# Performance work log

Hardware: AMD Instinct MI355X
Metric: run time of the kernel (lower is better)

Reference implementation:

```python
import jax, jax.numpy as jnp
import numpy as np

N, F_IN, F_OUT = 8192, 512, 64
LEAKY_ALPHA = 0.2
NEG_MASK = -9e15


def setup_inputs() -> dict:
    key = jax.random.key(0)
    k1, k2, k3, k4 = jax.random.split(key, 4)
    x = jax.random.normal(k1, (N, F_IN), dtype=jnp.float32)
    adj = jax.random.randint(k2, (N, N), 0, 2, dtype=jnp.int32)
    # xavier-normal-ish scale for params
    W = jax.random.normal(k3, (F_IN, F_OUT), dtype=jnp.float32) * np.sqrt(2.0 / (F_IN + F_OUT)).astype(np.float32)
    a = jax.random.normal(k4, (2 * F_OUT, 1), dtype=jnp.float32) * np.sqrt(2.0 / (2 * F_OUT + 1)).astype(np.float32)
    return {"x": x, "adj": adj, "W": W, "a": a}


def reference(x, adj, W, a):
    # eval mode: dropout is identity
    Wh = x @ W                                   # [N, F_out]
    wh_i = Wh @ a[:F_OUT, :]                     # [N, 1]
    wh_j = Wh @ a[F_OUT:, :]                     # [N, 1]
    e = wh_i + wh_j.T                            # [N, N] broadcast add
    e = jnp.where(e >= 0, e, LEAKY_ALPHA * e)    # leaky_relu
    e = jnp.where(adj > 0, e, NEG_MASK)
    attn = jax.nn.softmax(e, axis=1)             # row-wise softmax
    h = attn @ Wh                                # [N, F_out]
    # ELU activation
    return jax.nn.elu(h)
```

## Files before the change

### kernel.cpp

```cpp
#include <hip/hip_runtime.h>

#define NN 8192
#define FIN 512
#define FO 64

typedef short bf16x8 __attribute__((ext_vector_type(8)));
typedef float f32x4 __attribute__((ext_vector_type(4)));

union AFrag { bf16x8 v; __bf16 b[8]; };

__device__ __forceinline__ unsigned spread8(unsigned u) {
    u = (u | (u << 12)) & 0x000F000Fu;
    u = (u | (u << 6))  & 0x03030303u;
    u = (u | (u << 3))  & 0x11111111u;
    return u;
}

__global__ __launch_bounds__(512) void wt_kernel(const float* __restrict__ W, __bf16* __restrict__ WT) {
    __shared__ float tile[64][65];
    const int k0 = blockIdx.x * 64;
    #pragma unroll
    for (int r = 0; r < 8; ++r) {
        const int kl = r * 8 + (threadIdx.x >> 6);
        const int f  = threadIdx.x & 63;
        tile[kl][f] = W[(size_t)(k0 + kl) * FO + f];
    }
    __syncthreads();
    const int f   = threadIdx.x >> 3;
    const int kk8 = (threadIdx.x & 7) * 8;
    unsigned u[4];
    #pragma unroll
    for (int h = 0; h < 4; ++h) {
        union { __bf16 b; unsigned short us; } lo, hi;
        lo.b = (__bf16)tile[kk8 + 2*h][f];
        hi.b = (__bf16)tile[kk8 + 2*h + 1][f];
        u[h] = (unsigned)lo.us | ((unsigned)hi.us << 16);
    }
    *(uint4*)(WT + (size_t)f * FIN + k0 + kk8) = make_uint4(u[0], u[1], u[2], u[3]);
}

__global__ __launch_bounds__(128) void wh_kernel(
    const float* __restrict__ x, const __bf16* __restrict__ WT,
    const float* __restrict__ a, uint4* __restrict__ whs,
    float* __restrict__ s_out, float* __restrict__ t_out)
{
    __shared__ float whlds[2][16][FO + 1];
    const int w  = threadIdx.x >> 6;
    const int l  = threadIdx.x & 63;
    const int lr = l & 15, lg = l >> 4;
    const int rb = (blockIdx.x * 2 + w) * 16;

    f32x4 acc[4] = {};
    const float* xr = x + (size_t)(rb + lr) * FIN;
    const __bf16* wbase[4];
    #pragma unroll
    for (int ft = 0; ft < 4; ++ft) wbase[ft] = WT + (ft*16 + lr) * FIN;

    float4 nxa = *(const float4*)(xr + lg*4);
    float4 nxb = *(const float4*)(xr + lg*4 + 16);
    for (int ks = 0; ks < 16; ++ks) {
        const int k0 = ks*32 + lg*4;
        const float4 xa = nxa, xb = nxb;
        const int kn = (ks < 15 ? ks + 1 : 15)*32 + lg*4;
        nxa = *(const float4*)(xr + kn);
        nxb = *(const float4*)(xr + kn + 16);
        AFrag af;
        af.b[0]=(__bf16)xa.x; af.b[1]=(__bf16)xa.y; af.b[2]=(__bf16)xa.z; af.b[3]=(__bf16)xa.w;
        af.b[4]=(__bf16)xb.x; af.b[5]=(__bf16)xb.y; af.b[6]=(__bf16)xb.z; af.b[7]=(__bf16)xb.w;
        #pragma unroll
        for (int ft = 0; ft < 4; ++ft) {
            union { bf16x8 v; uint2 q[2]; } bf;
            bf.q[0] = *(const uint2*)(wbase[ft] + k0);
            bf.q[1] = *(const uint2*)(wbase[ft] + k0 + 16);
            acc[ft] = __builtin_amdgcn_mfma_f32_16x16x32_bf16(af.v, bf.v, acc[ft], 0, 0, 0);
        }
    }

    #pragma unroll
    for (int ft = 0; ft < 4; ++ft)
        #pragma unroll
        for (int q = 0; q < 4; ++q)
            whlds[w][lg*4+q][ft*16+lr] = acc[ft][q];

    float sp[4] = {0,0,0,0}, tp[4] = {0,0,0,0};
    #pragma unroll
    for (int ft = 0; ft < 4; ++ft) {
        const float a1 = a[ft*16 + lr];
        const float a2 = a[FO + ft*16 + lr];
        #pragma unroll
        for (int q = 0; q < 4; ++q) { sp[q] += acc[ft][q]*a1; tp[q] += acc[ft][q]*a2; }
    }
    #pragma unroll
    for (int d = 1; d < 16; d <<= 1) {
        #pragma unroll
        for (int q = 0; q < 4; ++q) { sp[q] += __shfl_xor(sp[q], d); tp[q] += __shfl_xor(tp[q], d); }
    }
    if (lr == 0) {
        *(float4*)(s_out + rb + lg*4) = make_float4(sp[0], sp[1], sp[2], sp[3]);
        *(float4*)(t_out + rb + lg*4) = make_float4(tp[0], tp[1], tp[2], tp[3]);
    }

    __syncthreads();

    const int jb = blockIdx.x;
    #pragma unroll
    for (int q = 0; q < 2; ++q) {
        const int ft = w*2 + q;
        const int f  = ft*16 + lr;
        unsigned u[4];
        #pragma unroll
        for (int h = 0; h < 4; ++h) {
            const int c0 = ((h & 2) ? 16 : 0) + lg*4 + (h & 1)*2;
            union { __bf16 b; unsigned short us; } lo, hi;
            lo.b = (__bf16)whlds[c0 >> 4][c0 & 15][f];
            hi.b = (__bf16)whlds[(c0+1) >> 4][(c0+1) & 15][f];
            u[h] = (unsigned)lo.us | ((unsigned)hi.us << 16);
        }
        whs[(jb*4 + ft)*64 + l] = make_uint4(u[0], u[1], u[2], u[3]);
    }
}

__global__ __launch_bounds__(256) void mask_kernel(
    const int* __restrict__ adj, unsigned* __restrict__ mask)
{
    const int l   = threadIdx.x & 63;
    const int wid = (blockIdx.x * 256 + threadIdx.x) >> 6;
    const int lsh = (l & 7) * 8;
    #pragma unroll 2
    for (int g = wid; g < NN * 32; g += 16384) {
        const int4 v = *(const int4*)(adj + (size_t)g * 256 + l * 4);
        const unsigned long long b0 = __ballot(v.x != 0);
        const unsigned long long b1 = __ballot(v.y != 0);
        const unsigned long long b2 = __ballot(v.z != 0);
        const unsigned long long b3 = __ballot(v.w != 0);
        if (l < 8) {
            const unsigned w0 = spread8((unsigned)(b0 >> lsh) & 0xFFu);
            const unsigned w1 = spread8((unsigned)(b1 >> lsh) & 0xFFu);
            const unsigned w2 = spread8((unsigned)(b2 >> lsh) & 0xFFu);
            const unsigned w3 = spread8((unsigned)(b3 >> lsh) & 0xFFu);
            mask[(size_t)g * 8 + l] = w0 | (w1 << 1) | (w2 << 2) | (w3 << 3);
        }
    }
}

__global__ __launch_bounds__(1024, 4) void gat3_kernel(
    const unsigned* __restrict__ mask, const uint4* __restrict__ whs,
    const float* __restrict__ s_in, const float* __restrict__ t_in,
    float* __restrict__ out)
{
    __shared__ float red[8][2048];
    __shared__ float dnl[16][32];
    __shared__ float dns[32];
    const int w  = threadIdx.x >> 6;
    const int l  = threadIdx.x & 63;
    const int lr = l & 15, lg = l >> 4;
    const int rg = blockIdx.x;
    const int r0 = rg * 32;
    const float sA = s_in[r0 + lr];
    const float sB = s_in[r0 + 16 + lr];
    const unsigned* mrowA = mask + (size_t)(r0 + lr) * 256;
    const unsigned* mrowB = mask + (size_t)(r0 + 16 + lr) * 256;
    const int sh0 = lg * 4;
    const bf16x8* wv = (const bf16x8*)whs;

    f32x4 acc[2][4] = {};
    float dnA = 0.f, dnB = 0.f;

    unsigned mA = mrowA[w*16], mB = mrowB[w*16];
    float4 t0 = *(const float4*)(t_in + w*512 + sh0);
    float4 t1 = *(const float4*)(t_in + w*512 + 16 + sh0);

    for (int it = 0; it < 16; ++it) {
        const int jb = w*16 + it;
        bf16x8 bv0 = wv[(jb*4 + 0)*64 + l];
        bf16x8 bv1 = wv[(jb*4 + 1)*64 + l];
        bf16x8 bv2 = wv[(jb*4 + 2)*64 + l];
        bf16x8 bv3 = wv[(jb*4 + 3)*64 + l];
        const int jn = w*16 + (it + 1 < 16 ? it + 1 : 15);
        const unsigned nmA = mrowA[jn], nmB = mrowB[jn];
        const float4 nt0 = *(const float4*)(t_in + jn*32 + sh0);
        const float4 nt1 = *(const float4*)(t_in + jn*32 + 16 + sh0);

        const float tv[8] = {t0.x, t0.y, t0.z, t0.w, t1.x, t1.y, t1.z, t1.w};
        AFrag afA, afB;
        #pragma unroll
        for (int e = 0; e < 8; ++e) {
            const int bit = (e < 4) ? (sh0 + e) : (12 + sh0 + e);
            float eA = sA + tv[e]; eA = fmaxf(eA, 0.2f * eA);
            float eB = sB + tv[e]; eB = fmaxf(eB, 0.2f * eB);
            const float pA = ((mA >> bit) & 1u) ? __expf(eA) : 0.f;
            const float pB = ((mB >> bit) & 1u) ? __expf(eB) : 0.f;
            dnA += pA; dnB += pB;
            afA.b[e] = (__bf16)pA;
            afB.b[e] = (__bf16)pB;
        }
        acc[0][0] = __builtin_amdgcn_mfma_f32_16x16x32_bf16(afA.v, bv0, acc[0][0], 0, 0, 0);
        acc[0][1] = __builtin_amdgcn_mfma_f32_16x16x32_bf16(afA.v, bv1, acc[0][1], 0, 0, 0);
        acc[0][2] = __builtin_amdgcn_mfma_f32_16x16x32_bf16(afA.v, bv2, acc[0][2], 0, 0, 0);
        acc[0][3] = __builtin_amdgcn_mfma_f32_16x16x32_bf16(afA.v, bv3, acc[0][3], 0, 0, 0);
        acc[1][0] = __builtin_amdgcn_mfma_f32_16x16x32_bf16(afB.v, bv0, acc[1][0], 0, 0, 0);
        acc[1][1] = __builtin_amdgcn_mfma_f32_16x16x32_bf16(afB.v, bv1, acc[1][1], 0, 0, 0);
        acc[1][2] = __builtin_amdgcn_mfma_f32_16x16x32_bf16(afB.v, bv2, acc[1][2], 0, 0, 0);
        acc[1][3] = __builtin_amdgcn_mfma_f32_16x16x32_bf16(afB.v, bv3, acc[1][3], 0, 0, 0);

        mA = nmA; mB = nmB; t0 = nt0; t1 = nt1;
    }

    dnA += __shfl_xor(dnA, 16); dnA += __shfl_xor(dnA, 32);
    dnB += __shfl_xor(dnB, 16); dnB += __shfl_xor(dnB, 32);
    if (l < 16) { dnl[w][l] = dnA; dnl[w][16 + l] = dnB; }
    __syncthreads();
    if (threadIdx.x < 32) {
        float s = 0.f;
        #pragma unroll
        for (int ww = 0; ww < 16; ++ww) s += dnl[ww][threadIdx.x];
        dns[threadIdx.x] = s;
    }

    for (int h = 8; h >= 1; h >>= 1) {
        if (w >= h && w < 2*h) {
            #pragma unroll
            for (int g = 0; g < 2; ++g)
                #pragma unroll
                for (int ft = 0; ft < 4; ++ft)
                    #pragma unroll
                    for (int q = 0; q < 4; ++q)
                        red[w - h][((g*16 + lg*4 + q)*FO) + ft*16 + lr] = acc[g][ft][q];
        }
        __syncthreads();
        if (w < h) {
            #pragma unroll
            for (int g = 0; g < 2; ++g)
                #pragma unroll
                for (int ft = 0; ft < 4; ++ft)
                    #pragma unroll
                    for (int q = 0; q < 4; ++q)
                        acc[g][ft][q] += red[w][((g*16 + lg*4 + q)*FO) + ft*16 + lr];
        }
        __syncthreads();
    }

    if (w == 0) {
        #pragma unroll
        for (int g = 0; g < 2; ++g) {
            #pragma unroll
            for (int ft = 0; ft < 4; ++ft) {
                #pragma unroll
                for (int q = 0; q < 4; ++q) {
                    const int m = g*16 + lg*4 + q;
                    const float h2 = acc[g][ft][q] / dns[m];
                    out[(size_t)(r0 + m) * FO + ft*16 + lr] =
                        (h2 > 0.f) ? h2 : (__expf(h2) - 1.f);
                }
            }
        }
    }
}

extern "C" void kernel_launch(void* const* d_in, const int* in_sizes, int n_in,
                              void* d_out, int out_size, void* d_ws, size_t ws_size,
                              hipStream_t stream) {
    const float* x   = (const float*)d_in[0];
    const int*   adj = (const int*)d_in[1];
    const float* W   = (const float*)d_in[2];
    const float* a   = (const float*)d_in[3];
    float* out = (float*)d_out;

    char* ws = (char*)d_ws;
    uint4*    whs  = (uint4*)ws;
    __bf16*   WT   = (__bf16*)(ws + (1u << 20));
    float*    s    = (float*)(ws + (1u << 20) + (1u << 16));
    float*    t    = (float*)(ws + (1u << 20) + (1u << 16) + 32768);
    unsigned* mask = (unsigned*)(ws + (2u << 20));

    wt_kernel  <<<8,    512, 0, stream>>>(W, WT);
    wh_kernel  <<<256,  128, 0, stream>>>(x, WT, a, whs, s, t);
    mask_kernel<<<4096, 256, 0, stream>>>(adj, mask);
    gat3_kernel<<<256, 1024, 0, stream>>>(mask, whs, s, t, out);
}
```

Measured before the change: 100.5 us.

## Fuse W transpose, Wh projection and adjacency mask packing into one launch

Removes the separate W-transpose kernel and merges the Wh GEMM kernel and the adj-to-bitmask kernel into one grid. The first 128 blocks compute Wh with 4 waves each, reading W directly from fp32 global memory and converting it to bf16 on the fly. The remaining 4096 blocks pack the mask, so the two independent stages overlap and two launches disappear. In exchange, the GEMM now does strided scalar W loads instead of vectorised loads of a pre-transposed bf16 copy.

Result: faster. 89.77 us (-10.6%).

```diff
diff --git a/kernel.cpp b/kernel.cpp
--- a/kernel.cpp
+++ b/kernel.cpp
@@ -16,45 +16,43 @@
     return u;
 }
 
-__global__ __launch_bounds__(512) void wt_kernel(const float* __restrict__ W, __bf16* __restrict__ WT) {
-    __shared__ float tile[64][65];
-    const int k0 = blockIdx.x * 64;
-    #pragma unroll
-    for (int r = 0; r < 8; ++r) {
-        const int kl = r * 8 + (threadIdx.x >> 6);
-        const int f  = threadIdx.x & 63;
-        tile[kl][f] = W[(size_t)(k0 + kl) * FO + f];
-    }
-    __syncthreads();
-    const int f   = threadIdx.x >> 3;
-    const int kk8 = (threadIdx.x & 7) * 8;
-    unsigned u[4];
-    #pragma unroll
-    for (int h = 0; h < 4; ++h) {
-        union { __bf16 b; unsigned short us; } lo, hi;
-        lo.b = (__bf16)tile[kk8 + 2*h][f];
-        hi.b = (__bf16)tile[kk8 + 2*h + 1][f];
-        u[h] = (unsigned)lo.us | ((unsigned)hi.us << 16);
-    }
-    *(uint4*)(WT + (size_t)f * FIN + k0 + kk8) = make_uint4(u[0], u[1], u[2], u[3]);
-}
-
-__global__ __launch_bounds__(128) void wh_kernel(
-    const float* __restrict__ x, const __bf16* __restrict__ WT,
+__global__ __launch_bounds__(256, 5) void fat_kernel(
+    const int* __restrict__ adj, unsigned* __restrict__ mask,
+    const float* __restrict__ x, const float* __restrict__ W,
     const float* __restrict__ a, uint4* __restrict__ whs,
     float* __restrict__ s_out, float* __restrict__ t_out)
 {
-    __shared__ float whlds[2][16][FO + 1];
+    __shared__ float whlds[4][16][FO + 1];
+    const int l  = threadIdx.x & 63;
+
+    if (blockIdx.x >= 128) {
+        const int mb  = blockIdx.x - 128;
+        const int wid = (mb * 256 + (int)threadIdx.x) >> 6;
+        const int lsh = (l & 7) * 8;
+        #pragma unroll 4
+        for (int g = wid; g < NN * 32; g += 16384) {
+            const int4 v = *(const int4*)(adj + (size_t)g * 256 + l * 4);
+            const unsigned long long b0 = __ballot(v.x != 0);
+            const unsigned long long b1 = __ballot(v.y != 0);
+            const unsigned long long b2 = __ballot(v.z != 0);
+            const unsigned long long b3 = __ballot(v.w != 0);
+            if (l < 8) {
+                const unsigned w0 = spread8((unsigned)(b0 >> lsh) & 0xFFu);
+                const unsigned w1 = spread8((unsigned)(b1 >> lsh) & 0xFFu);
+                const unsigned w2 = spread8((unsigned)(b2 >> lsh) & 0xFFu);
+                const unsigned w3 = spread8((unsigned)(b3 >> lsh) & 0xFFu);
+                mask[(size_t)g * 8 + l] = w0 | (w1 << 1) | (w2 << 2) | (w3 << 3);
+            }
+        }
+        return;
+    }
+
     const int w  = threadIdx.x >> 6;
-    const int l  = threadIdx.x & 63;
     const int lr = l & 15, lg = l >> 4;
-    const int rb = (blockIdx.x * 2 + w) * 16;
+    const int rb = (blockIdx.x * 4 + w) * 16;
 
     f32x4 acc[4] = {};
     const float* xr = x + (size_t)(rb + lr) * FIN;
-    const __bf16* wbase[4];
-    #pragma unroll
-    for (int ft = 0; ft < 4; ++ft) wbase[ft] = WT + (ft*16 + lr) * FIN;
 
     float4 nxa = *(const float4*)(xr + lg*4);
     float4 nxb = *(const float4*)(xr + lg*4 + 16);
@@ -69,9 +67,13 @@
         af.b[4]=(__bf16)xb.x; af.b[5]=(__bf16)xb.y; af.b[6]=(__bf16)xb.z; af.b[7]=(__bf16)xb.w;
         #pragma unroll
         for (int ft = 0; ft < 4; ++ft) {
-            union { bf16x8 v; uint2 q[2]; } bf;
-            bf.q[0] = *(const uint2*)(wbase[ft] + k0);
-            bf.q[1] = *(const uint2*)(wbase[ft] + k0 + 16);
+            const int f = ft*16 + lr;
+            AFrag bf;
+            #pragma unroll
+            for (int j = 0; j < 4; ++j) {
+                bf.b[j]     = (__bf16)W[(size_t)(k0 + j) * FO + f];
+                bf.b[4 + j] = (__bf16)W[(size_t)(k0 + 16 + j) * FO + f];
+            }
             acc[ft] = __builtin_amdgcn_mfma_f32_16x16x32_bf16(af.v, bf.v, acc[ft], 0, 0, 0);
         }
     }
@@ -102,44 +104,23 @@
 
     __syncthreads();
 
-    const int jb = blockIdx.x;
+    const int half = w >> 1;
+    const int wp   = w & 1;
+    const int jb   = blockIdx.x * 2 + half;
     #pragma unroll
     for (int q = 0; q < 2; ++q) {
-        const int ft = w*2 + q;
+        const int ft = wp*2 + q;
         const int f  = ft*16 + lr;
         unsigned u[4];
         #pragma unroll
         for (int h = 0; h < 4; ++h) {
             const int c0 = ((h & 2) ? 16 : 0) + lg*4 + (h & 1)*2;
             union { __bf16 b; unsigned short us; } lo, hi;
-            lo.b = (__bf16)whlds[c0 >> 4][c0 & 15][f];
-            hi.b = (__bf16)whlds[(c0+1) >> 4][(c0+1) & 15][f];
+            lo.b = (__bf16)whlds[half*2 + (c0 >> 4)][c0 & 15][f];
+            hi.b = (__bf16)whlds[half*2 + ((c0+1) >> 4)][(c0+1) & 15][f];
             u[h] = (unsigned)lo.us | ((unsigned)hi.us << 16);
         }
         whs[(jb*4 + ft)*64 + l] = make_uint4(u[0], u[1], u[2], u[3]);
-    }
-}
-
-__global__ __launch_bounds__(256) void mask_kernel(
-    const int* __restrict__ adj, unsigned* __restrict__ mask)
-{
-    const int l   = threadIdx.x & 63;
-    const int wid = (blockIdx.x * 256 + threadIdx.x) >> 6;
-    const int lsh = (l & 7) * 8;
-    #pragma unroll 2
-    for (int g = wid; g < NN * 32; g += 16384) {
-        const int4 v = *(const int4*)(adj + (size_t)g * 256 + l * 4);
-        const unsigned long long b0 = __ballot(v.x != 0);
-        const unsigned long long b1 = __ballot(v.y != 0);
-        const unsigned long long b2 = __ballot(v.z != 0);
-        const unsigned long long b3 = __ballot(v.w != 0);
-        if (l < 8) {
-            const unsigned w0 = spread8((unsigned)(b0 >> lsh) & 0xFFu);
-            const unsigned w1 = spread8((unsigned)(b1 >> lsh) & 0xFFu);
-            const unsigned w2 = spread8((unsigned)(b2 >> lsh) & 0xFFu);
-            const unsigned w3 = spread8((unsigned)(b3 >> lsh) & 0xFFu);
-            mask[(size_t)g * 8 + l] = w0 | (w1 << 1) | (w2 << 2) | (w3 << 3);
-        }
     }
 }
 
@@ -268,13 +249,10 @@
 
     char* ws = (char*)d_ws;
     uint4*    whs  = (uint4*)ws;
-    __bf16*   WT   = (__bf16*)(ws + (1u << 20));
     float*    s    = (float*)(ws + (1u << 20) + (1u << 16));
     float*    t    = (float*)(ws + (1u << 20) + (1u << 16) + 32768);
     unsigned* mask = (unsigned*)(ws + (2u << 20));
 
-    wt_kernel  <<<8,    512, 0, stream>>>(W, WT);
-    wh_kernel  <<<256,  128, 0, stream>>>(x, WT, a, whs, s, t);
-    mask_kernel<<<4096, 256, 0, stream>>>(adj, mask);
+    fat_kernel <<<4224, 256, 0, stream>>>(adj, mask, x, W, a, whs, s, t);
     gat3_kernel<<<256, 1024, 0, stream>>>(mask, whs, s, t, out);
 }
```
